# Optimization experiments

Measured on AMD Instinct MI355X. Metric: run time of the kernel, lower is better.

The kernel has to match this reference:

```python
import jax, jax.numpy as jnp
import numpy as np

EMB_DIM = 1024
N_EXPERTS = 8
TOP_K = 2
MOE_HIDDEN = 1024
NORM_TOPK = True


def setup_inputs() -> dict:
    key = jax.random.key(0)
    ks = jax.random.split(key, 7)
    s = 0.02
    return {
        "x": jax.random.normal(ks[0], (2, 2048, EMB_DIM), dtype=jnp.float32),
        "router_w": jax.random.normal(ks[1], (N_EXPERTS, EMB_DIM), dtype=jnp.float32) * s,
        "router_b": jnp.zeros((N_EXPERTS,), dtype=jnp.float32),
        "gate_up_w": jax.random.normal(ks[2], (N_EXPERTS, 2 * MOE_HIDDEN, EMB_DIM), dtype=jnp.float32) * s,
        "gate_up_b": jnp.zeros((N_EXPERTS, 2 * MOE_HIDDEN), dtype=jnp.float32),
        "down_w": jax.random.normal(ks[3], (N_EXPERTS, EMB_DIM, MOE_HIDDEN), dtype=jnp.float32) * s,
        "down_b": jnp.zeros((N_EXPERTS, EMB_DIM), dtype=jnp.float32),
    }


def _swiglu(h):
    # SwiGLUFFN: even columns gate, odd columns up
    gate = h[:, ::2]
    up = h[:, 1::2]
    return jnp.clip(gate, -7.0, 7.0) * jax.nn.sigmoid(1.702 * gate) * (jnp.clip(up, -7.0, 7.0) + 1.0)


def reference(x, router_w, router_b, gate_up_w, gate_up_b, down_w, down_b):
    B, S, D = x.shape
    h = x.reshape(B * S, D)  # [T, D]
    # Router: linear -> top-k -> (softmax over k)
    scores = h @ router_w.T + router_b  # [T, E]
    vals, idx = jax.lax.top_k(scores, TOP_K)  # [T, K]
    if NORM_TOPK:
        vals = jax.nn.softmax(vals, axis=-1)
    # Combine weights per (token, expert); zero for unselected experts, so
    # masked-dense compute below is mathematically identical to gather/scatter.
    cw = jnp.sum(jax.nn.one_hot(idx, N_EXPERTS, dtype=vals.dtype) * vals[..., None], axis=1)  # [T, E]
    out = jnp.zeros_like(h)
    for e in range(N_EXPERTS):  # fixed small expert count
        g = h @ gate_up_w[e].T + gate_up_b[e]  # [T, 2H]
        a = _swiglu(g)  # [T, H]
        oe = a @ down_w[e].T + down_b[e]  # [T, D]
        out = out + oe * cw[:, e:e + 1]
    return out.reshape(B, S, D)
```

## Files before the change

kernel.cpp:

```cpp
#include <hip/hip_runtime.h>
#include <hip/hip_bf16.h>

#define EMB 1024
#define NEXP 8
#define NH 1024
#define N_GU 2048
#define TOPK 2

#define BM 128
#define BN 128
#define BK 64
#define KTILES 16
#define MAXTILES 72

typedef __attribute__((ext_vector_type(4))) float f32x4;
typedef __attribute__((ext_vector_type(8))) short s16x8;
typedef __attribute__((ext_vector_type(4))) short s16x4;

typedef __attribute__((address_space(3))) unsigned int lds_u32;
typedef __attribute__((address_space(1))) const unsigned int glb_u32;

__device__ __forceinline__ void gl_lds16(const void* g, void* l) {
  __builtin_amdgcn_global_load_lds((glb_u32*)g, (lds_u32*)l, 16, 0, 0);
}

__device__ __forceinline__ unsigned short f2bf(float f) {
  union { float f; unsigned int u; } a; a.f = f;
  unsigned int u = a.u;
  unsigned int r = (u + 0x7FFFu + ((u >> 16) & 1u)) >> 16;
  return (unsigned short)r;
}

__device__ __forceinline__ int xcd_swz(int bid, int nwg) {
  int q = nwg >> 3, r = nwg & 7;
  int xcd = bid & 7, pos = bid >> 3;
  int base = (xcd < r) ? xcd * (q + 1) : r * (q + 1) + (xcd - r) * q;
  return base + pos;
}

__global__ void convert_all(const float* __restrict__ a, unsigned short* __restrict__ oa, int n4a,
                            const float* __restrict__ b, unsigned short* __restrict__ ob, int n4b,
                            const float* __restrict__ c, unsigned short* __restrict__ oc, int n4c) {
  int tot = n4a + n4b + n4c;
  for (int i = blockIdx.x * blockDim.x + threadIdx.x; i < tot; i += gridDim.x * blockDim.x) {
    const float* src; unsigned short* dst; int k;
    if (i < n4a) { src = a; dst = oa; k = i; }
    else if (i < n4a + n4b) { src = b; dst = ob; k = i - n4a; }
    else { src = c; dst = oc; k = i - n4a - n4b; }
    float4 v = ((const float4*)src)[k];
    s16x4 o;
    o[0] = (short)f2bf(v.x);
    o[1] = (short)f2bf(v.y);
    o[2] = (short)f2bf(v.z);
    o[3] = (short)f2bf(v.w);
    ((s16x4*)dst)[k] = o;
  }
}

__global__ void router_topk(const float* __restrict__ x, const float* __restrict__ rw,
                            const float* __restrict__ rb, int T,
                            int* __restrict__ tokE, float* __restrict__ tokW) {
  int gwid = (blockIdx.x * blockDim.x + threadIdx.x) >> 6;
  int lane = threadIdx.x & 63;
  if (gwid >= T) return;
  const float* h = x + (size_t)gwid * EMB;
  float hreg[16];
  #pragma unroll
  for (int i = 0; i < 16; ++i) hreg[i] = h[lane + 64 * i];
  float sc[NEXP];
  #pragma unroll
  for (int e = 0; e < NEXP; ++e) {
    const float* w = rw + e * EMB;
    float s = 0.f;
    #pragma unroll
    for (int i = 0; i < 16; ++i) s += hreg[i] * w[lane + 64 * i];
    #pragma unroll
    for (int off = 32; off > 0; off >>= 1) s += __shfl_xor(s, off);
    sc[e] = s + rb[e];
  }
  if (lane == 0) {
    int e0 = 0; float v0 = sc[0];
    #pragma unroll
    for (int e = 1; e < NEXP; ++e) if (sc[e] > v0) { v0 = sc[e]; e0 = e; }
    int e1 = -1; float v1 = -3.0e38f;
    #pragma unroll
    for (int e = 0; e < NEXP; ++e) { if (e == e0) continue; if (sc[e] > v1) { v1 = sc[e]; e1 = e; } }
    float ex = __expf(v1 - v0);
    float w0 = 1.f / (1.f + ex);
    float w1 = ex / (1.f + ex);
    tokE[gwid * 2] = e0; tokE[gwid * 2 + 1] = e1;
    tokW[gwid * 2] = w0; tokW[gwid * 2 + 1] = w1;
  }
}

__global__ void count_meta(const int* __restrict__ tokE, int A,
                           int* __restrict__ offsets, int* __restrict__ tilemeta) {
  __shared__ int hist[NEXP];
  int t = threadIdx.x;
  if (t < NEXP) hist[t] = 0;
  __syncthreads();
  for (int i = t; i < A; i += blockDim.x) atomicAdd(&hist[tokE[i]], 1);
  __syncthreads();
  if (t == 0) {
    int off = 0, nt = 0;
    for (int e = 0; e < NEXP; ++e) {
      offsets[e] = off;
      int c = hist[e];
      int ntile = (c + BM - 1) / BM;
      for (int k = 0; k < ntile; ++k) {
        tilemeta[1 + nt * 3 + 0] = e;
        tilemeta[1 + nt * 3 + 1] = off + k * BM;
        tilemeta[1 + nt * 3 + 2] = off + c;
        nt++;
      }
      off += c;
    }
    offsets[NEXP] = off;
    tilemeta[0] = nt;
  }
}

__global__ void scatter_tokens(const int* __restrict__ tokE, const int* __restrict__ offsets,
                               int* __restrict__ fill, int* __restrict__ rows,
                               int* __restrict__ apos, int A) {
  int i = blockIdx.x * blockDim.x + threadIdx.x;
  int lane = threadIdx.x & 63;
  int e = tokE[i];
  int p = -1;
  #pragma unroll
  for (int ex = 0; ex < NEXP; ++ex) {
    unsigned long long mask = __ballot(e == ex);
    if (mask) {
      int leader = __ffsll(mask) - 1;
      int cnt = __popcll(mask);
      int base = 0;
      if (lane == leader) base = atomicAdd(&fill[ex], cnt);
      base = __shfl(base, leader);
      if (e == ex) {
        int rank = __popcll(mask & ((1ull << lane) - 1ull));
        p = offsets[ex] + base + rank;
      }
    }
  }
  rows[p] = i >> 1;
  apos[i] = p;
}

__global__ __launch_bounds__(256, 4) void gemm_gate_up(
    const unsigned short* __restrict__ xb,
    const unsigned short* __restrict__ gub,
    const float* __restrict__ gu_bias,
    const int* __restrict__ rows,
    const int* __restrict__ tilemeta,
    unsigned short* __restrict__ hact) {
  __shared__ __align__(16) short As[BM * BK];
  __shared__ __align__(16) short Bs[BN * BK];
  int wg = xcd_swz(blockIdx.x, gridDim.x);
  int tileid = wg >> 4;
  int n0 = (wg & 15) * BN;
  int nt = tilemeta[0];
  if (tileid >= nt) return;
  int e    = tilemeta[1 + tileid * 3 + 0];
  int m0   = tilemeta[1 + tileid * 3 + 1];
  int mEnd = tilemeta[1 + tileid * 3 + 2];

  int t = threadIdx.x;
  int lane = t & 63;
  int wid = t >> 6;
  int wr = wid >> 1, wc = wid & 1;

  int srow = lane >> 3;
  int scol = (((lane & 7) ^ (srow & 7)) * 8);
  const unsigned short* ga[4];
  const unsigned short* gb[4];
  int dstoff[4];
  #pragma unroll
  for (int q = 0; q < 4; ++q) {
    int rt = wid * 32 + q * 8 + srow;
    int ai = m0 + rt; if (ai >= mEnd) ai = mEnd - 1;
    ga[q] = xb + (size_t)rows[ai] * EMB + scol;
    gb[q] = gub + ((size_t)e * N_GU + n0 + rt) * EMB + scol;
    dstoff[q] = (wid * 32 + q * 8) * BK;
  }

  int fr = lane & 15;
  int q8 = (lane >> 4) * 8;
  int rsw = (fr & 7) << 3;

  f32x4 acc[4][4];
  #pragma unroll
  for (int i = 0; i < 4; ++i)
    #pragma unroll
    for (int j = 0; j < 4; ++j) acc[i][j] = (f32x4){0.f, 0.f, 0.f, 0.f};

  for (int tk = 0; tk < KTILES; ++tk) {
    int k0 = tk * BK;
    __syncthreads();
    #pragma unroll
    for (int q = 0; q < 4; ++q) {
      gl_lds16(ga[q] + k0, &As[dstoff[q]]);
      gl_lds16(gb[q] + k0, &Bs[dstoff[q]]);
    }
    __syncthreads();
    #pragma unroll
    for (int kk = 0; kk < BK; kk += 32) {
      s16x8 a[4], b[4];
      #pragma unroll
      for (int i = 0; i < 4; ++i)
        a[i] = *(const s16x8*)(&As[(wr * 64 + i * 16 + fr) * BK + ((kk + q8) ^ rsw)]);
      #pragma unroll
      for (int j = 0; j < 4; ++j)
        b[j] = *(const s16x8*)(&Bs[(wc * 64 + j * 16 + fr) * BK + ((kk + q8) ^ rsw)]);
      #pragma unroll
      for (int i = 0; i < 4; ++i)
        #pragma unroll
        for (int j = 0; j < 4; ++j)
          acc[i][j] = __builtin_amdgcn_mfma_f32_16x16x32_bf16(a[i], b[j], acc[i][j], 0, 0, 0);
    }
  }

  const float* bias_e = gu_bias + (size_t)e * N_GU;
  int rbase = m0 + wr * 64 + ((lane >> 4) * 4);
  #pragma unroll
  for (int i = 0; i < 4; ++i) {
    #pragma unroll
    for (int j = 0; j < 4; ++j) {
      int n = n0 + wc * 64 + j * 16 + fr;
      float v[4], o[4];
      #pragma unroll
      for (int r = 0; r < 4; ++r) v[r] = acc[i][j][r] + bias_e[n];
      #pragma unroll
      for (int r = 0; r < 4; ++r) o[r] = __shfl_xor(v[r], 1);
      if ((lane & 1) == 0) {
        int outc = n >> 1;
        #pragma unroll
        for (int r = 0; r < 4; ++r) {
          int pos = rbase + i * 16 + r;
          if (pos < mEnd) {
            float g = v[r], u = o[r];
            float gc = fminf(fmaxf(g, -7.f), 7.f);
            float uc = fminf(fmaxf(u, -7.f), 7.f);
            float sig = 1.f / (1.f + __expf(-1.702f * g));
            float act = gc * sig * (uc + 1.f);
            hact[(size_t)pos * NH + outc] = f2bf(act);
          }
        }
      }
    }
  }
}

__global__ __launch_bounds__(256, 4) void gemm_down(
    const unsigned short* __restrict__ hact,
    const unsigned short* __restrict__ dwb,
    const int* __restrict__ tilemeta,
    float* __restrict__ y) {
  __shared__ __align__(16) short As[BM * BK];
  __shared__ __align__(16) short Bs[BN * BK];
  int wg = xcd_swz(blockIdx.x, gridDim.x);
  int tileid = wg >> 3;
  int n0 = (wg & 7) * BN;
  int nt = tilemeta[0];
  if (tileid >= nt) return;
  int e    = tilemeta[1 + tileid * 3 + 0];
  int m0   = tilemeta[1 + tileid * 3 + 1];
  int mEnd = tilemeta[1 + tileid * 3 + 2];

  int t = threadIdx.x;
  int lane = t & 63;
  int wid = t >> 6;
  int wr = wid >> 1, wc = wid & 1;

  int srow = lane >> 3;
  int scol = (((lane & 7) ^ (srow & 7)) * 8);
  const unsigned short* ga[4];
  const unsigned short* gb[4];
  int dstoff[4];
  #pragma unroll
  for (int q = 0; q < 4; ++q) {
    int rt = wid * 32 + q * 8 + srow;
    int ai = m0 + rt; if (ai >= mEnd) ai = mEnd - 1;
    ga[q] = hact + (size_t)ai * NH + scol;
    gb[q] = dwb + ((size_t)e * EMB + n0 + rt) * NH + scol;
    dstoff[q] = (wid * 32 + q * 8) * BK;
  }

  int fr = lane & 15;
  int q8 = (lane >> 4) * 8;
  int rsw = (fr & 7) << 3;

  f32x4 acc[4][4];
  #pragma unroll
  for (int i = 0; i < 4; ++i)
    #pragma unroll
    for (int j = 0; j < 4; ++j) acc[i][j] = (f32x4){0.f, 0.f, 0.f, 0.f};

  for (int tk = 0; tk < KTILES; ++tk) {
    int k0 = tk * BK;
    __syncthreads();
    #pragma unroll
    for (int q = 0; q < 4; ++q) {
      gl_lds16(ga[q] + k0, &As[dstoff[q]]);
      gl_lds16(gb[q] + k0, &Bs[dstoff[q]]);
    }
    __syncthreads();
    #pragma unroll
    for (int kk = 0; kk < BK; kk += 32) {
      s16x8 a[4], b[4];
      #pragma unroll
      for (int i = 0; i < 4; ++i)
        a[i] = *(const s16x8*)(&As[(wr * 64 + i * 16 + fr) * BK + ((kk + q8) ^ rsw)]);
      #pragma unroll
      for (int j = 0; j < 4; ++j)
        b[j] = *(const s16x8*)(&Bs[(wc * 64 + j * 16 + fr) * BK + ((kk + q8) ^ rsw)]);
      #pragma unroll
      for (int i = 0; i < 4; ++i)
        #pragma unroll
        for (int j = 0; j < 4; ++j)
          acc[i][j] = __builtin_amdgcn_mfma_f32_16x16x32_bf16(a[i], b[j], acc[i][j], 0, 0, 0);
    }
  }

  int rbase = m0 + wr * 64 + ((lane >> 4) * 4);
  #pragma unroll
  for (int i = 0; i < 4; ++i) {
    #pragma unroll
    for (int j = 0; j < 4; ++j) {
      int n = n0 + wc * 64 + j * 16 + fr;
      #pragma unroll
      for (int r = 0; r < 4; ++r) {
        int pos = rbase + i * 16 + r;
        if (pos < mEnd) y[(size_t)pos * EMB + n] = acc[i][j][r];
      }
    }
  }
}

__global__ void combine_out(const float* __restrict__ y, const float* __restrict__ down_b,
                            const int* __restrict__ tokE, const float* __restrict__ tokW,
                            const int* __restrict__ apos, float* __restrict__ out, int T) {
  int i = blockIdx.x * blockDim.x + threadIdx.x;
  int tot = T * (EMB / 4);
  if (i >= tot) return;
  int tok = i >> 8;
  int c = i & 255;
  int e0 = tokE[tok * 2], e1 = tokE[tok * 2 + 1];
  float w0 = tokW[tok * 2], w1 = tokW[tok * 2 + 1];
  int p0 = apos[tok * 2], p1 = apos[tok * 2 + 1];
  float4 y0 = ((const float4*)(y + (size_t)p0 * EMB))[c];
  float4 y1 = ((const float4*)(y + (size_t)p1 * EMB))[c];
  float4 b0 = ((const float4*)(down_b + (size_t)e0 * EMB))[c];
  float4 b1 = ((const float4*)(down_b + (size_t)e1 * EMB))[c];
  float4 o;
  o.x = w0 * (y0.x + b0.x) + w1 * (y1.x + b1.x);
  o.y = w0 * (y0.y + b0.y) + w1 * (y1.y + b1.y);
  o.z = w0 * (y0.z + b0.z) + w1 * (y1.z + b1.z);
  o.w = w0 * (y0.w + b0.w) + w1 * (y1.w + b1.w);
  ((float4*)out)[i] = o;
}

extern "C" void kernel_launch(void* const* d_in, const int* in_sizes, int n_in,
                              void* d_out, int out_size, void* d_ws, size_t ws_size,
                              hipStream_t stream) {
  const float* x   = (const float*)d_in[0];
  const float* rw  = (const float*)d_in[1];
  const float* rb  = (const float*)d_in[2];
  const float* guw = (const float*)d_in[3];
  const float* gub = (const float*)d_in[4];
  const float* dw  = (const float*)d_in[5];
  const float* db  = (const float*)d_in[6];
  float* out = (float*)d_out;

  int T = in_sizes[0] / EMB;
  int A = T * TOPK;

  char* ws = (char*)d_ws;
  size_t off = 0;
  auto alloc = [&](size_t bytes) -> void* {
    void* p = ws + off;
    off = (off + bytes + 255) & ~((size_t)255);
    return p;
  };
  unsigned short* xb   = (unsigned short*)alloc((size_t)T * EMB * 2);
  unsigned short* guwb = (unsigned short*)alloc((size_t)NEXP * N_GU * EMB * 2);
  unsigned short* dwb  = (unsigned short*)alloc((size_t)NEXP * EMB * NH * 2);
  unsigned short* hact = (unsigned short*)alloc((size_t)A * NH * 2);
  float* y             = (float*)alloc((size_t)A * EMB * 4);
  int*   tokE    = (int*)alloc((size_t)A * 4);
  float* tokW    = (float*)alloc((size_t)A * 4);
  int*   apos    = (int*)alloc((size_t)A * 4);
  int*   rowsArr = (int*)alloc((size_t)A * 4);
  int*   fill    = (int*)alloc(NEXP * 4);
  int*   offsets = (int*)alloc((NEXP + 1) * 4);
  int*   tilemeta= (int*)alloc((1 + MAXTILES * 3) * 4);

  hipMemsetAsync(fill, 0, NEXP * 4, stream);

  int n4x = T * EMB / 4;
  int n4g = NEXP * N_GU * EMB / 4;
  int n4d = NEXP * EMB * NH / 4;
  convert_all<<<2048, 256, 0, stream>>>(x, xb, n4x, guw, guwb, n4g, dw, dwb, n4d);

  router_topk<<<T / 4, 256, 0, stream>>>(x, rw, rb, T, tokE, tokW);
  count_meta<<<1, 1024, 0, stream>>>(tokE, A, offsets, tilemeta);
  scatter_tokens<<<A / 256, 256, 0, stream>>>(tokE, offsets, fill, rowsArr, apos, A);

  gemm_gate_up<<<MAXTILES * (N_GU / BN), 256, 0, stream>>>(xb, guwb, gub, rowsArr, tilemeta, hact);
  gemm_down<<<MAXTILES * (EMB / BN), 256, 0, stream>>>(hact, dwb, tilemeta, y);

  combine_out<<<(T * EMB / 4 + 255) / 256, 256, 0, stream>>>(y, db, tokE, tokW, apos, out, T);
}
```

Baseline: 159.1 us.

## Fuse weighted combine into down GEMM epilogue via atomic scatter-add

The down-projection GEMM now adds the bias, scales by the routing weight and atomically accumulates into the token's output row. This removes the intermediate per-assignment y buffer and the separate combine kernel. scatter_tokens now writes per-slot weights instead of assignment positions, and the output is zeroed with a memset first. The cost is float atomics with scattered addressing and nondeterministic summation order.

After: 173.5 us. +9.0%, slower.

```diff
diff --git a/kernel.cpp b/kernel.cpp
--- a/kernel.cpp
+++ b/kernel.cpp
@@ -120,9 +120,10 @@
   }
 }
 
-__global__ void scatter_tokens(const int* __restrict__ tokE, const int* __restrict__ offsets,
+__global__ void scatter_tokens(const int* __restrict__ tokE, const float* __restrict__ tokW,
+                               const int* __restrict__ offsets,
                                int* __restrict__ fill, int* __restrict__ rows,
-                               int* __restrict__ apos, int A) {
+                               float* __restrict__ wgt, int A) {
   int i = blockIdx.x * blockDim.x + threadIdx.x;
   int lane = threadIdx.x & 63;
   int e = tokE[i];
@@ -143,7 +144,7 @@
     }
   }
   rows[p] = i >> 1;
-  apos[i] = p;
+  wgt[p] = tokW[i];
 }
 
 __global__ __launch_bounds__(256, 4) void gemm_gate_up(
@@ -253,8 +254,11 @@
 __global__ __launch_bounds__(256, 4) void gemm_down(
     const unsigned short* __restrict__ hact,
     const unsigned short* __restrict__ dwb,
+    const float* __restrict__ down_b,
+    const int* __restrict__ rows,
+    const float* __restrict__ wgt,
     const int* __restrict__ tilemeta,
-    float* __restrict__ y) {
+    float* __restrict__ out) {
   __shared__ __align__(16) short As[BM * BK];
   __shared__ __align__(16) short Bs[BN * BK];
   int wg = xcd_swz(blockIdx.x, gridDim.x);
@@ -321,42 +325,31 @@
     }
   }
 
+  const float* bias_e = down_b + (size_t)e * EMB;
   int rbase = m0 + wr * 64 + ((lane >> 4) * 4);
   #pragma unroll
   for (int i = 0; i < 4; ++i) {
+    int pb = rbase + i * 16;
+    int tok[4]; float w4[4];
+    #pragma unroll
+    for (int r = 0; r < 4; ++r) {
+      int pos = pb + r;
+      int cp = (pos < mEnd) ? pos : (mEnd - 1);
+      tok[r] = rows[cp];
+      w4[r] = wgt[cp];
+    }
     #pragma unroll
     for (int j = 0; j < 4; ++j) {
       int n = n0 + wc * 64 + j * 16 + fr;
+      float b = bias_e[n];
       #pragma unroll
       for (int r = 0; r < 4; ++r) {
-        int pos = rbase + i * 16 + r;
-        if (pos < mEnd) y[(size_t)pos * EMB + n] = acc[i][j][r];
+        int pos = pb + r;
+        if (pos < mEnd)
+          atomicAdd(&out[(size_t)tok[r] * EMB + n], w4[r] * (acc[i][j][r] + b));
       }
     }
   }
-}
-
-__global__ void combine_out(const float* __restrict__ y, const float* __restrict__ down_b,
-                            const int* __restrict__ tokE, const float* __restrict__ tokW,
-                            const int* __restrict__ apos, float* __restrict__ out, int T) {
-  int i = blockIdx.x * blockDim.x + threadIdx.x;
-  int tot = T * (EMB / 4);
-  if (i >= tot) return;
-  int tok = i >> 8;
-  int c = i & 255;
-  int e0 = tokE[tok * 2], e1 = tokE[tok * 2 + 1];
-  float w0 = tokW[tok * 2], w1 = tokW[tok * 2 + 1];
-  int p0 = apos[tok * 2], p1 = apos[tok * 2 + 1];
-  float4 y0 = ((const float4*)(y + (size_t)p0 * EMB))[c];
-  float4 y1 = ((const float4*)(y + (size_t)p1 * EMB))[c];
-  float4 b0 = ((const float4*)(down_b + (size_t)e0 * EMB))[c];
-  float4 b1 = ((const float4*)(down_b + (size_t)e1 * EMB))[c];
-  float4 o;
-  o.x = w0 * (y0.x + b0.x) + w1 * (y1.x + b1.x);
-  o.y = w0 * (y0.y + b0.y) + w1 * (y1.y + b1.y);
-  o.z = w0 * (y0.z + b0.z) + w1 * (y1.z + b1.z);
-  o.w = w0 * (y0.w + b0.w) + w1 * (y1.w + b1.w);
-  ((float4*)out)[i] = o;
 }
 
 extern "C" void kernel_launch(void* const* d_in, const int* in_sizes, int n_in,
@@ -385,16 +378,16 @@
   unsigned short* guwb = (unsigned short*)alloc((size_t)NEXP * N_GU * EMB * 2);
   unsigned short* dwb  = (unsigned short*)alloc((size_t)NEXP * EMB * NH * 2);
   unsigned short* hact = (unsigned short*)alloc((size_t)A * NH * 2);
-  float* y             = (float*)alloc((size_t)A * EMB * 4);
   int*   tokE    = (int*)alloc((size_t)A * 4);
   float* tokW    = (float*)alloc((size_t)A * 4);
-  int*   apos    = (int*)alloc((size_t)A * 4);
   int*   rowsArr = (int*)alloc((size_t)A * 4);
+  float* wgtArr  = (float*)alloc((size_t)A * 4);
   int*   fill    = (int*)alloc(NEXP * 4);
   int*   offsets = (int*)alloc((NEXP + 1) * 4);
   int*   tilemeta= (int*)alloc((1 + MAXTILES * 3) * 4);
 
   hipMemsetAsync(fill, 0, NEXP * 4, stream);
+  hipMemsetAsync(out, 0, (size_t)T * EMB * 4, stream);
 
   int n4x = T * EMB / 4;
   int n4g = NEXP * N_GU * EMB / 4;
@@ -403,10 +396,8 @@
 
   router_topk<<<T / 4, 256, 0, stream>>>(x, rw, rb, T, tokE, tokW);
   count_meta<<<1, 1024, 0, stream>>>(tokE, A, offsets, tilemeta);
-  scatter_tokens<<<A / 256, 256, 0, stream>>>(tokE, offsets, fill, rowsArr, apos, A);
+  scatter_tokens<<<A / 256, 256, 0, stream>>>(tokE, tokW, offsets, fill, rowsArr, wgtArr, A);
 
   gemm_gate_up<<<MAXTILES * (N_GU / BN), 256, 0, stream>>>(xb, guwb, gub, rowsArr, tilemeta, hact);
-  gemm_down<<<MAXTILES * (EMB / BN), 256, 0, stream>>>(hact, dwb, tilemeta, y);
-
-  combine_out<<<(T * EMB / 4 + 255) / 256, 256, 0, stream>>>(y, db, tokE, tokW, apos, out, T);
-}
+  gemm_down<<<MAXTILES * (EMB / BN), 256, 0, stream>>>(hact, dwb, db, rowsArr, wgtArr, tilemeta, out);
+}
```

## Enlarge gate-up GEMM tiles to 256x256 with 512-thread blocks

Applied to the files above, without the earlier changes.

The gate_up GEMM moves from 128x128 tiles with 4 waves to 256x256 tiles with 8 waves, each wave computing a 128x64 sub-tile. count_meta now builds two tile-metadata tables, one with 256-row tiles for gate_up and one with 128-row tiles for down. Larger tiles raise arithmetic intensity and cut redundant reloads of A and B from global memory. In exchange, each block uses more registers and LDS, fewer blocks fill the GPU, and more rows are wasted as padding in partially filled expert tiles.

After: 200.3 us. 1.26x slower.

```diff
diff --git a/kernel.cpp b/kernel.cpp
--- a/kernel.cpp
+++ b/kernel.cpp
@@ -7,11 +7,16 @@
 #define N_GU 2048
 #define TOPK 2
 
-#define BM 128
-#define BN 128
 #define BK 64
 #define KTILES 16
-#define MAXTILES 72
+
+#define BMg 256
+#define BNg 256
+#define MAXT256 40
+
+#define BMd 128
+#define BNd 128
+#define MAXT128 72
 
 typedef __attribute__((ext_vector_type(4))) float f32x4;
 typedef __attribute__((ext_vector_type(8))) short s16x8;
@@ -94,7 +99,8 @@
 }
 
 __global__ void count_meta(const int* __restrict__ tokE, int A,
-                           int* __restrict__ offsets, int* __restrict__ tilemeta) {
+                           int* __restrict__ offsets,
+                           int* __restrict__ tm256, int* __restrict__ tm128) {
   __shared__ int hist[NEXP];
   int t = threadIdx.x;
   if (t < NEXP) hist[t] = 0;
@@ -102,21 +108,29 @@
   for (int i = t; i < A; i += blockDim.x) atomicAdd(&hist[tokE[i]], 1);
   __syncthreads();
   if (t == 0) {
-    int off = 0, nt = 0;
+    int off = 0, nt2 = 0, nt1 = 0;
     for (int e = 0; e < NEXP; ++e) {
       offsets[e] = off;
       int c = hist[e];
-      int ntile = (c + BM - 1) / BM;
-      for (int k = 0; k < ntile; ++k) {
-        tilemeta[1 + nt * 3 + 0] = e;
-        tilemeta[1 + nt * 3 + 1] = off + k * BM;
-        tilemeta[1 + nt * 3 + 2] = off + c;
-        nt++;
+      int n2 = (c + BMg - 1) / BMg;
+      for (int k = 0; k < n2; ++k) {
+        tm256[1 + nt2 * 3 + 0] = e;
+        tm256[1 + nt2 * 3 + 1] = off + k * BMg;
+        tm256[1 + nt2 * 3 + 2] = off + c;
+        nt2++;
+      }
+      int n1 = (c + BMd - 1) / BMd;
+      for (int k = 0; k < n1; ++k) {
+        tm128[1 + nt1 * 3 + 0] = e;
+        tm128[1 + nt1 * 3 + 1] = off + k * BMd;
+        tm128[1 + nt1 * 3 + 2] = off + c;
+        nt1++;
       }
       off += c;
     }
     offsets[NEXP] = off;
-    tilemeta[0] = nt;
+    tm256[0] = nt2;
+    tm128[0] = nt1;
   }
 }
 
@@ -146,18 +160,18 @@
   apos[i] = p;
 }
 
-__global__ __launch_bounds__(256, 4) void gemm_gate_up(
+__global__ __launch_bounds__(512, 2) void gemm_gate_up(
     const unsigned short* __restrict__ xb,
     const unsigned short* __restrict__ gub,
     const float* __restrict__ gu_bias,
     const int* __restrict__ rows,
     const int* __restrict__ tilemeta,
     unsigned short* __restrict__ hact) {
-  __shared__ __align__(16) short As[BM * BK];
-  __shared__ __align__(16) short Bs[BN * BK];
+  __shared__ __align__(16) short As[BMg * BK];
+  __shared__ __align__(16) short Bs[BNg * BK];
   int wg = xcd_swz(blockIdx.x, gridDim.x);
-  int tileid = wg >> 4;
-  int n0 = (wg & 15) * BN;
+  int tileid = wg >> 3;
+  int n0 = (wg & 7) * BNg;
   int nt = tilemeta[0];
   if (tileid >= nt) return;
   int e    = tilemeta[1 + tileid * 3 + 0];
@@ -167,7 +181,8 @@
   int t = threadIdx.x;
   int lane = t & 63;
   int wid = t >> 6;
-  int wr = wid >> 1, wc = wid & 1;
+  int wr = wid >> 2;
+  int wc = wid & 3;
 
   int srow = lane >> 3;
   int scol = (((lane & 7) ^ (srow & 7)) * 8);
@@ -176,20 +191,20 @@
   int dstoff[4];
   #pragma unroll
   for (int q = 0; q < 4; ++q) {
-    int rt = wid * 32 + q * 8 + srow;
+    int rt = q * 64 + wid * 8 + srow;
     int ai = m0 + rt; if (ai >= mEnd) ai = mEnd - 1;
     ga[q] = xb + (size_t)rows[ai] * EMB + scol;
     gb[q] = gub + ((size_t)e * N_GU + n0 + rt) * EMB + scol;
-    dstoff[q] = (wid * 32 + q * 8) * BK;
+    dstoff[q] = (q * 64 + wid * 8) * BK;
   }
 
   int fr = lane & 15;
   int q8 = (lane >> 4) * 8;
   int rsw = (fr & 7) << 3;
 
-  f32x4 acc[4][4];
-  #pragma unroll
-  for (int i = 0; i < 4; ++i)
+  f32x4 acc[8][4];
+  #pragma unroll
+  for (int i = 0; i < 8; ++i)
     #pragma unroll
     for (int j = 0; j < 4; ++j) acc[i][j] = (f32x4){0.f, 0.f, 0.f, 0.f};
 
@@ -204,15 +219,15 @@
     __syncthreads();
     #pragma unroll
     for (int kk = 0; kk < BK; kk += 32) {
-      s16x8 a[4], b[4];
-      #pragma unroll
-      for (int i = 0; i < 4; ++i)
-        a[i] = *(const s16x8*)(&As[(wr * 64 + i * 16 + fr) * BK + ((kk + q8) ^ rsw)]);
+      s16x8 a[8], b[4];
+      #pragma unroll
+      for (int i = 0; i < 8; ++i)
+        a[i] = *(const s16x8*)(&As[(wr * 128 + i * 16 + fr) * BK + ((kk + q8) ^ rsw)]);
       #pragma unroll
       for (int j = 0; j < 4; ++j)
         b[j] = *(const s16x8*)(&Bs[(wc * 64 + j * 16 + fr) * BK + ((kk + q8) ^ rsw)]);
       #pragma unroll
-      for (int i = 0; i < 4; ++i)
+      for (int i = 0; i < 8; ++i)
         #pragma unroll
         for (int j = 0; j < 4; ++j)
           acc[i][j] = __builtin_amdgcn_mfma_f32_16x16x32_bf16(a[i], b[j], acc[i][j], 0, 0, 0);
@@ -220,9 +235,9 @@
   }
 
   const float* bias_e = gu_bias + (size_t)e * N_GU;
-  int rbase = m0 + wr * 64 + ((lane >> 4) * 4);
-  #pragma unroll
-  for (int i = 0; i < 4; ++i) {
+  int rbase = m0 + wr * 128 + ((lane >> 4) * 4);
+  #pragma unroll
+  for (int i = 0; i < 8; ++i) {
     #pragma unroll
     for (int j = 0; j < 4; ++j) {
       int n = n0 + wc * 64 + j * 16 + fr;
@@ -255,11 +270,11 @@
     const unsigned short* __restrict__ dwb,
     const int* __restrict__ tilemeta,
     float* __restrict__ y) {
-  __shared__ __align__(16) short As[BM * BK];
-  __shared__ __align__(16) short Bs[BN * BK];
+  __shared__ __align__(16) short As[BMd * BK];
+  __shared__ __align__(16) short Bs[BNd * BK];
   int wg = xcd_swz(blockIdx.x, gridDim.x);
   int tileid = wg >> 3;
-  int n0 = (wg & 7) * BN;
+  int n0 = (wg & 7) * BNd;
   int nt = tilemeta[0];
   if (tileid >= nt) return;
   int e    = tilemeta[1 + tileid * 3 + 0];
@@ -392,7 +407,8 @@
   int*   rowsArr = (int*)alloc((size_t)A * 4);
   int*   fill    = (int*)alloc(NEXP * 4);
   int*   offsets = (int*)alloc((NEXP + 1) * 4);
-  int*   tilemeta= (int*)alloc((1 + MAXTILES * 3) * 4);
+  int*   tm256   = (int*)alloc((1 + MAXT256 * 3) * 4);
+  int*   tm128   = (int*)alloc((1 + MAXT128 * 3) * 4);
 
   hipMemsetAsync(fill, 0, NEXP * 4, stream);
 
@@ -402,11 +418,11 @@
   convert_all<<<2048, 256, 0, stream>>>(x, xb, n4x, guw, guwb, n4g, dw, dwb, n4d);
 
   router_topk<<<T / 4, 256, 0, stream>>>(x, rw, rb, T, tokE, tokW);
-  count_meta<<<1, 1024, 0, stream>>>(tokE, A, offsets, tilemeta);
+  count_meta<<<1, 1024, 0, stream>>>(tokE, A, offsets, tm256, tm128);
   scatter_tokens<<<A / 256, 256, 0, stream>>>(tokE, offsets, fill, rowsArr, apos, A);
 
-  gemm_gate_up<<<MAXTILES * (N_GU / BN), 256, 0, stream>>>(xb, guwb, gub, rowsArr, tilemeta, hact);
-  gemm_down<<<MAXTILES * (EMB / BN), 256, 0, stream>>>(hact, dwb, tilemeta, y);
+  gemm_gate_up<<<MAXT256 * (N_GU / BNg), 512, 0, stream>>>(xb, guwb, gub, rowsArr, tm256, hact);
+  gemm_down<<<MAXT128 * (EMB / BNd), 256, 0, stream>>>(hact, dwb, tm128, y);
 
   combine_out<<<(T * EMB / 4 + 255) / 256, 256, 0, stream>>>(y, db, tokE, tokW, apos, out, T);
 }
```
